# Optimization experiments

Hardware: AMD Instinct MI355X
Metric: run time of the kernel (lower is better)

Reference implementation:

```python
import jax, jax.numpy as jnp
import numpy as np

B, T, C, H = 2, 2048, 1024, 16
D = C // H  # head_dim = 64

def setup_inputs() -> dict:
    key = jax.random.key(0)
    k0, k1, k2, k3, k4 = jax.random.split(key, 5)
    s = 1.0 / np.sqrt(C)
    return {
        "x": jax.random.normal(k0, (B, T, C), dtype=jnp.float32),
        "w_qkv": jax.random.uniform(k1, (C, 3 * C), jnp.float32, -s, s),
        "b_qkv": jax.random.uniform(k2, (3 * C,), jnp.float32, -s, s),
        "w_proj": jax.random.uniform(k3, (C, C), jnp.float32, -s, s),
        "b_proj": jax.random.uniform(k4, (C,), jnp.float32, -s, s),
    }

def reference(x, w_qkv, b_qkv, w_proj, b_proj):
    Bx, Tx, Cx = x.shape
    qkv = x @ w_qkv + b_qkv                      # [B,T,3C]
    q, k, v = jnp.split(qkv, 3, axis=-1)
    # [B,T,C] -> [B,H,T,D]
    def heads(t):
        return t.reshape(Bx, Tx, H, D).transpose(0, 2, 1, 3)
    q, k, v = heads(q), heads(k), heads(v)
    att = jnp.einsum('bhqd,bhkd->bhqk', q, k) / np.sqrt(D).astype(np.float32)
    causal = jnp.tril(jnp.ones((Tx, Tx), dtype=bool))
    att = jnp.where(causal, att, -jnp.inf)
    att = jax.nn.softmax(att, axis=-1)
    y = jnp.einsum('bhqk,bhkd->bhqd', att, v)    # [B,H,T,D]
    y = y.transpose(0, 2, 1, 3).reshape(Bx, Tx, Cx)
    return y @ w_proj + b_proj
```

## Files before the change

kernel.cpp:

```cpp
#include <hip/hip_runtime.h>

typedef short bf16x8 __attribute__((ext_vector_type(8)));
typedef float f32x4 __attribute__((ext_vector_type(4)));
typedef unsigned short u16;
typedef unsigned short u16x8 __attribute__((ext_vector_type(8)));
typedef unsigned short u16x4 __attribute__((ext_vector_type(4), may_alias));
typedef float f32x4_a __attribute__((ext_vector_type(4), may_alias));

__device__ __forceinline__ u16 f2bf(float f) {
    union { float f; unsigned u; } v; v.f = f;
    unsigned r = v.u + 0x7fffu + ((v.u >> 16) & 1u);
    return (u16)(r >> 16);
}
__device__ __forceinline__ u16 f2bf_rhu(float f) {
    union { float f; unsigned u; } v; v.f = f;
    return (u16)((v.u + 0x8000u) >> 16);
}

__device__ __forceinline__ void gld_lds16(const void* g, void* l) {
    __builtin_amdgcn_global_load_lds(
        (const __attribute__((address_space(1))) void*)g,
        (__attribute__((address_space(3))) void*)l, 16, 0, 0);
}

__global__ __launch_bounds__(256) void prep_kernel(
    const float* __restrict__ x, u16* __restrict__ xb,
    const float* __restrict__ w_qkv, u16* __restrict__ wqkvT,
    const float* __restrict__ w_proj, u16* __restrict__ wprojT) {
    __shared__ float tile[32][33];
    const int b = blockIdx.x, tid = threadIdx.x;
    if (b < 2048) {
        const int i = b * 256 + tid;
        float4 a = ((const float4*)x)[i * 2];
        float4 c = ((const float4*)x)[i * 2 + 1];
        u16x8 h;
        h[0] = f2bf(a.x); h[1] = f2bf(a.y); h[2] = f2bf(a.z); h[3] = f2bf(a.w);
        h[4] = f2bf(c.x); h[5] = f2bf(c.y); h[6] = f2bf(c.z); h[7] = f2bf(c.w);
        *(u16x8*)(xb + (size_t)i * 8) = h;
        return;
    }
    const float* in; u16* out; int N, bx;
    if (b < 5120) { bx = b - 2048; in = w_qkv; out = wqkvT; N = 3072; }
    else          { bx = b - 5120; in = w_proj; out = wprojT; N = 1024; }
    const int nblk = N / 32;
    const int n0 = (bx % nblk) * 32, k0 = (bx / nblk) * 32;
    const int tx = tid & 31, ty = tid >> 5;
#pragma unroll
    for (int i = 0; i < 32; i += 8)
        tile[ty + i][tx] = in[(size_t)(k0 + ty + i) * N + n0 + tx];
    __syncthreads();
#pragma unroll
    for (int i = 0; i < 32; i += 8)
        out[(size_t)(n0 + ty + i) * 1024 + k0 + tx] = f2bf(tile[tx][ty + i]);
}

#define QSCALE 0.180336880f

template <int OUTMODE, int BN>
__global__ __launch_bounds__(256) void gemm_m97(
    const u16* __restrict__ A, const u16* __restrict__ Bt,
    const float* __restrict__ bias, float* __restrict__ Cf,
    u16* __restrict__ Qo, u16* __restrict__ Ko, u16* __restrict__ Vt,
    int M, int N, int K) {
    constexpr int NF = BN / 32;
    __shared__ __align__(16) u16 lA[128 * 64];
    __shared__ __align__(16) u16 lB[BN * 64];

    const int tid = threadIdx.x;
    const int lane = tid & 63, wid = tid >> 6;
    const int wr = wid >> 1, wc = wid & 1;
    const int fr = lane & 15, fq = lane >> 4;
    const int m0 = blockIdx.y * 128, n0 = blockIdx.x * BN;

    const int gsrc = (lane & 7) ^ (lane >> 3);
    const u16* gA0 = A + (size_t)(m0 + (tid >> 3)) * K + gsrc * 8;
    const u16* gB0 = Bt + (size_t)(n0 + (tid >> 3)) * K + gsrc * 8;
    u16* lAw = lA + wid * 512;
    u16* lBw = lB + wid * 512;

    const int r7 = fr & 7;
    const int gk[2] = { ((0 + fq) ^ r7) * 8, ((4 + fq) ^ r7) * 8 };

    f32x4 acc[4][NF];
#pragma unroll
    for (int m = 0; m < 4; m++)
#pragma unroll
        for (int n = 0; n < NF; n++)
#pragma unroll
            for (int r = 0; r < 4; r++) acc[m][n][r] = 0.f;

    for (int k0 = 0; k0 < K; k0 += 64) {
        __syncthreads();
#pragma unroll
        for (int c = 0; c < 4; c++)
            gld_lds16(gA0 + (size_t)(c * 32) * K + k0, lAw + c * 2048);
#pragma unroll
        for (int c = 0; c < BN / 32; c++)
            gld_lds16(gB0 + (size_t)(c * 32) * K + k0, lBw + c * 2048);
        __syncthreads();

#pragma unroll
        for (int kf = 0; kf < 2; kf++) {
            bf16x8 a[4], b[NF];
#pragma unroll
            for (int m = 0; m < 4; m++)
                a[m] = *(const bf16x8*)&lA[(wr * 64 + m * 16 + fr) * 64 + gk[kf]];
#pragma unroll
            for (int n = 0; n < NF; n++)
                b[n] = *(const bf16x8*)&lB[(wc * (BN / 2) + n * 16 + fr) * 64 + gk[kf]];
#pragma unroll
            for (int m = 0; m < 4; m++)
#pragma unroll
                for (int n = 0; n < NF; n++)
                    acc[m][n] = __builtin_amdgcn_mfma_f32_16x16x32_bf16(a[m], b[n], acc[m][n], 0, 0, 0);
        }
    }

#pragma unroll
    for (int m = 0; m < 4; m++) {
#pragma unroll
        for (int n = 0; n < NF; n++) {
            const int row0 = m0 + wr * 64 + m * 16 + fq * 4;
            const int col = n0 + wc * (BN / 2) + n * 16 + fr;
            float v4[4];
#pragma unroll
            for (int r = 0; r < 4; r++) v4[r] = acc[m][n][r] + bias[col];
            if (OUTMODE == 0) {
                const int bb = row0 >> 11, t0 = row0 & 2047;
                const int sec = col >> 10, cc = col & 1023;
                const int h = cc >> 6, d = cc & 63;
                if (sec == 0) {
#pragma unroll
                    for (int r = 0; r < 4; r++)
                        Qo[(((size_t)(bb * 16 + h) * 2048 + t0 + r) << 6) + d] = f2bf(v4[r] * QSCALE);
                } else if (sec == 1) {
#pragma unroll
                    for (int r = 0; r < 4; r++)
                        Ko[(((size_t)(bb * 16 + h) * 2048 + t0 + r) << 6) + d] = f2bf(v4[r]);
                } else {
                    ushort4 p;
                    p.x = f2bf(v4[0]); p.y = f2bf(v4[1]); p.z = f2bf(v4[2]); p.w = f2bf(v4[3]);
                    *(ushort4*)&Vt[(((size_t)(bb * 16 + h) * 64 + d) << 11) + t0] = p;
                }
            } else {
#pragma unroll
                for (int r = 0; r < 4; r++)
                    Cf[(size_t)(row0 + r) * N + col] = v4[r];
            }
        }
    }
}

__global__ __launch_bounds__(256, 4) void attn_kernel(const u16* __restrict__ Q,
                                                      const u16* __restrict__ Kg,
                                                      const u16* __restrict__ Vt,
                                                      u16* __restrict__ O) {
    __shared__ __align__(16) u16 smem[16384];
    u16* lV = smem + 8192;
    u16* lPw;

    const int tid = threadIdx.x;
    const int lane = tid & 63, wid = tid >> 6;
    const int fr = lane & 15, fq = lane >> 4;
    const int kw = wid >> 1, qw = wid & 1;
    lPw = smem + 12288 + wid * 1024;
    const int bh = blockIdx.x & 31;
    const int qi = 31 - (blockIdx.x >> 5);
    const int qb0 = qi * 64;
    const size_t base = (size_t)bh * (2048 * 64);
    const u16* Qp = Q + base;
    const u16* Kp = Kg + base;
    const u16* Vp = Vt + base;

    const int q0w = qb0 + qw * 32;
    bf16x8 qa[2][2];
#pragma unroll
    for (int qg = 0; qg < 2; qg++)
#pragma unroll
        for (int kf = 0; kf < 2; kf++)
            qa[qg][kf] = *(const bf16x8*)&Qp[(size_t)(q0w + qg * 16 + fr) * 64 + kf * 32 + fq * 8];

    bf16x8 vones;
#pragma unroll
    for (int j = 0; j < 8; j++) vones[j] = (short)0x3F80;

    f32x4 o[4][2], lsum[2];
#pragma unroll
    for (int qg = 0; qg < 2; qg++) {
#pragma unroll
        for (int r = 0; r < 4; r++) lsum[qg][r] = 0.f;
#pragma unroll
        for (int dg = 0; dg < 4; dg++)
#pragma unroll
            for (int r = 0; r < 4; r++) o[dg][qg][r] = 0.f;
    }

    const int srow0 = wid * 8 + (lane >> 3);
    const int gsrc = (lane & 7) ^ (lane >> 3);
    const u16* kSrc0 = Kp + (size_t)srow0 * 64 + gsrc * 8;
    const u16* vSrc0 = Vp + ((size_t)srow0 << 11) + gsrc * 8;

    const int r7 = fr & 7;
    const int gk0 = ((0 + fq) ^ r7) * 8;
    const int gk1 = ((4 + fq) ^ r7) * 8;
    const int gkv = ((kw * 4 + fq) ^ r7) * 8;

    const int r4x = (fr & 3) ^ (fr >> 2);

    const int nt = qi + 1;

#define STAGE_K(bufofs, kt0_)                                                   \
    do {                                                                        \
        u16* _lkw = smem + (bufofs) + wid * 512;                                \
        gld_lds16(kSrc0 + (size_t)(kt0_) * 64, _lkw);                           \
        gld_lds16(kSrc0 + (size_t)((kt0_) + 32) * 64, _lkw + 2048);             \
    } while (0)
#define STAGE_V(kt0_)                                                           \
    do {                                                                        \
        u16* _lvw = lV + wid * 512;                                             \
        gld_lds16(vSrc0 + (kt0_), _lvw);                                        \
        gld_lds16(vSrc0 + ((size_t)32 << 11) + (kt0_), _lvw + 2048);            \
    } while (0)

    STAGE_K(0, 0);
    STAGE_V(0);
    asm volatile("s_waitcnt vmcnt(0)" ::: "memory");
    __builtin_amdgcn_s_barrier();

    for (int kt = 0; kt < nt; kt++) {
        const int kt0 = kt << 6;
        const int curofs = (kt & 1) ? 4096 : 0;

        if (kt + 1 < nt) {
            STAGE_K(curofs ^ 4096, kt0 + 64);
            asm volatile("s_waitcnt vmcnt(2)" ::: "memory");
            __builtin_amdgcn_s_barrier();
        } else if (nt > 1) {
            asm volatile("s_waitcnt vmcnt(0)" ::: "memory");
            __builtin_amdgcn_s_barrier();
        }
        const u16* lKc = smem + curofs;

        f32x4 s[2][2];
#pragma unroll
        for (int kg = 0; kg < 2; kg++)
#pragma unroll
            for (int qg = 0; qg < 2; qg++)
#pragma unroll
                for (int r = 0; r < 4; r++) s[kg][qg][r] = 0.f;
        __builtin_amdgcn_s_setprio(1);
#pragma unroll
        for (int kg = 0; kg < 2; kg++) {
            const int krow = (kw * 32 + kg * 16 + fr) * 64;
            bf16x8 kb0 = *(const bf16x8*)&lKc[krow + gk0];
            bf16x8 kb1 = *(const bf16x8*)&lKc[krow + gk1];
#pragma unroll
            for (int qg = 0; qg < 2; qg++) {
                s[kg][qg] = __builtin_amdgcn_mfma_f32_16x16x32_bf16(kb0, qa[qg][0], s[kg][qg], 0, 0, 0);
                s[kg][qg] = __builtin_amdgcn_mfma_f32_16x16x32_bf16(kb1, qa[qg][1], s[kg][qg], 0, 0, 0);
            }
        }
        __builtin_amdgcn_s_setprio(0);

        if (kt == nt - 1) {
#pragma unroll
            for (int kg = 0; kg < 2; kg++) {
                const int kg0 = kt0 + kw * 32 + kg * 16 + fq * 4;
#pragma unroll
                for (int qg = 0; qg < 2; qg++) {
                    const int qg0 = q0w + qg * 16 + fr;
#pragma unroll
                    for (int r = 0; r < 4; r++)
                        if (kg0 + r > qg0) s[kg][qg][r] = -200.f;
                }
            }
        }

#pragma unroll
        for (int kg = 0; kg < 2; kg++)
#pragma unroll
            for (int qg = 0; qg < 2; qg++) {
                const int ql = qg * 16 + fr;
                u16x4 w;
                w[0] = f2bf_rhu(__builtin_amdgcn_exp2f(s[kg][qg][0]));
                w[1] = f2bf_rhu(__builtin_amdgcn_exp2f(s[kg][qg][1]));
                w[2] = f2bf_rhu(__builtin_amdgcn_exp2f(s[kg][qg][2]));
                w[3] = f2bf_rhu(__builtin_amdgcn_exp2f(s[kg][qg][3]));
                const int g = (kg * 2 + (fq >> 1)) ^ r4x;
                *(u16x4*)&lPw[ql * 32 + g * 8 + (fq & 1) * 4] = w;
            }
        asm volatile("" ::: "memory");

        __builtin_amdgcn_s_setprio(1);
        bf16x8 va[4];
#pragma unroll
        for (int dg = 0; dg < 4; dg++)
            va[dg] = *(const bf16x8*)&lV[(dg * 16 + fr) * 64 + gkv];
#pragma unroll
        for (int qg = 0; qg < 2; qg++) {
            const int ql = qg * 16 + fr;
            bf16x8 pb = *(const bf16x8*)&lPw[ql * 32 + (fq ^ r4x) * 8];
            lsum[qg] = __builtin_amdgcn_mfma_f32_16x16x32_bf16(vones, pb, lsum[qg], 0, 0, 0);
#pragma unroll
            for (int dg = 0; dg < 4; dg++)
                o[dg][qg] = __builtin_amdgcn_mfma_f32_16x16x32_bf16(va[dg], pb, o[dg][qg], 0, 0, 0);
        }
        __builtin_amdgcn_s_setprio(0);

        if (kt + 1 < nt) {
            __builtin_amdgcn_s_barrier();
            STAGE_V(kt0 + 64);
        }
    }
#undef STAGE_K
#undef STAGE_V

    __syncthreads();

    float* cmb = (float*)smem;
    float* slab = cmb + (size_t)qw * 2560 + lane * 40;
    if (kw == 1) {
#pragma unroll
        for (int dg = 0; dg < 4; dg++)
#pragma unroll
            for (int qg = 0; qg < 2; qg++)
                *(f32x4_a*)&slab[(dg * 2 + qg) * 4] = o[dg][qg];
#pragma unroll
        for (int qg = 0; qg < 2; qg++)
            *(f32x4_a*)&slab[32 + qg * 4] = lsum[qg];
    }
    __syncthreads();
    if (kw == 0) {
#pragma unroll
        for (int dg = 0; dg < 4; dg++)
#pragma unroll
            for (int qg = 0; qg < 2; qg++) {
                f32x4_a p = *(const f32x4_a*)&slab[(dg * 2 + qg) * 4];
#pragma unroll
                for (int r = 0; r < 4; r++) o[dg][qg][r] += p[r];
            }
#pragma unroll
        for (int qg = 0; qg < 2; qg++) {
            f32x4_a p = *(const f32x4_a*)&slab[32 + qg * 4];
            lsum[qg][0] += p[0];
        }

        const int bb = bh >> 4, hh = bh & 15;
#pragma unroll
        for (int qg = 0; qg < 2; qg++) {
            const float inv = 1.f / lsum[qg][0];
            u16* orow = O + ((size_t)(bb * 2048 + q0w + qg * 16 + fr)) * 1024 + hh * 64 + fq * 4;
#pragma unroll
            for (int dg = 0; dg < 4; dg++) {
                ushort4 h;
                h.x = f2bf(o[dg][qg][0] * inv);
                h.y = f2bf(o[dg][qg][1] * inv);
                h.z = f2bf(o[dg][qg][2] * inv);
                h.w = f2bf(o[dg][qg][3] * inv);
                *(ushort4*)&orow[dg * 16] = h;
            }
        }
    }
}

extern "C" void kernel_launch(void* const* d_in, const int* in_sizes, int n_in,
                              void* d_out, int out_size, void* d_ws, size_t ws_size,
                              hipStream_t stream) {
    const float* x      = (const float*)d_in[0];
    const float* w_qkv  = (const float*)d_in[1];
    const float* b_qkv  = (const float*)d_in[2];
    const float* w_proj = (const float*)d_in[3];
    const float* b_proj = (const float*)d_in[4];
    float* out = (float*)d_out;

    u16* ws = (u16*)d_ws;
    u16* wqkvT  = ws;
    u16* wprojT = wqkvT + 3072 * 1024;
    u16* Qb     = wprojT + 1024 * 1024;
    u16* Kb     = Qb + 32 * 2048 * 64;
    u16* Vtb    = Kb + 32 * 2048 * 64;
    u16* xb     = Vtb + 32 * 2048 * 64;
    u16* attnO  = xb;

    prep_kernel<<<6144, 256, 0, stream>>>(x, xb, w_qkv, wqkvT, w_proj, wprojT);

    gemm_m97<0, 128><<<dim3(24, 32), 256, 0, stream>>>(
        xb, wqkvT, b_qkv, nullptr, Qb, Kb, Vtb, 4096, 3072, 1024);

    attn_kernel<<<1024, 256, 0, stream>>>(Qb, Kb, Vtb, attnO);

    gemm_m97<1, 64><<<dim3(16, 32), 256, 0, stream>>>(
        attnO, wprojT, b_proj, out, nullptr, nullptr, nullptr, 4096, 1024, 1024);
}
```

Baseline: 97.05 us.

## Build P operand with permlane swaps and move w_proj transpose into attention tail

The softmax probabilities are now repacked into the MFMA B-operand in registers using v_permlane32/16_swap instead of a round trip through per-wave LDS. This cuts LDS use from 32KB to 24KB, and launch bounds are raised to allow 5 blocks per CU. The w_proj transpose/convert moves out of the prep kernel into 1024 extra blocks appended to the attention launch, which shortens the prep kernel and fills the attention tail. The risks are extra permlane instructions, register pressure under the tighter occupancy bound, and the correctness of the lane permutation.

Measured after the change: 116.8 us. +20.3%, slower.

```diff
diff --git a/kernel.cpp b/kernel.cpp
--- a/kernel.cpp
+++ b/kernel.cpp
@@ -4,7 +4,6 @@
 typedef float f32x4 __attribute__((ext_vector_type(4)));
 typedef unsigned short u16;
 typedef unsigned short u16x8 __attribute__((ext_vector_type(8)));
-typedef unsigned short u16x4 __attribute__((ext_vector_type(4), may_alias));
 typedef float f32x4_a __attribute__((ext_vector_type(4), may_alias));
 
 __device__ __forceinline__ u16 f2bf(float f) {
@@ -25,8 +24,7 @@
 
 __global__ __launch_bounds__(256) void prep_kernel(
     const float* __restrict__ x, u16* __restrict__ xb,
-    const float* __restrict__ w_qkv, u16* __restrict__ wqkvT,
-    const float* __restrict__ w_proj, u16* __restrict__ wprojT) {
+    const float* __restrict__ w_qkv, u16* __restrict__ wqkvT) {
     __shared__ float tile[32][33];
     const int b = blockIdx.x, tid = threadIdx.x;
     if (b < 2048) {
@@ -39,19 +37,16 @@
         *(u16x8*)(xb + (size_t)i * 8) = h;
         return;
     }
-    const float* in; u16* out; int N, bx;
-    if (b < 5120) { bx = b - 2048; in = w_qkv; out = wqkvT; N = 3072; }
-    else          { bx = b - 5120; in = w_proj; out = wprojT; N = 1024; }
-    const int nblk = N / 32;
-    const int n0 = (bx % nblk) * 32, k0 = (bx / nblk) * 32;
+    const int bx = b - 2048;
+    const int n0 = (bx % 96) * 32, k0 = (bx / 96) * 32;
     const int tx = tid & 31, ty = tid >> 5;
 #pragma unroll
     for (int i = 0; i < 32; i += 8)
-        tile[ty + i][tx] = in[(size_t)(k0 + ty + i) * N + n0 + tx];
+        tile[ty + i][tx] = w_qkv[(size_t)(k0 + ty + i) * 3072 + n0 + tx];
     __syncthreads();
 #pragma unroll
     for (int i = 0; i < 32; i += 8)
-        out[(size_t)(n0 + ty + i) * 1024 + k0 + tx] = f2bf(tile[tx][ty + i]);
+        wqkvT[(size_t)(n0 + ty + i) * 1024 + k0 + tx] = f2bf(tile[tx][ty + i]);
 }
 
 #define QSCALE 0.180336880f
@@ -151,19 +146,35 @@
     }
 }
 
-__global__ __launch_bounds__(256, 4) void attn_kernel(const u16* __restrict__ Q,
+__global__ __launch_bounds__(256, 5) void attn_kernel(const u16* __restrict__ Q,
                                                       const u16* __restrict__ Kg,
                                                       const u16* __restrict__ Vt,
-                                                      u16* __restrict__ O) {
-    __shared__ __align__(16) u16 smem[16384];
+                                                      u16* __restrict__ O,
+                                                      const float* __restrict__ wp,
+                                                      u16* __restrict__ wpT) {
+    __shared__ __align__(16) u16 smem[12288];
+
+    const int tid = threadIdx.x;
+
+    if (blockIdx.x >= 1024) {
+        float* tile = (float*)smem;
+        const int bx = blockIdx.x - 1024;
+        const int n0 = (bx & 31) * 32, k0 = (bx >> 5) * 32;
+        const int tx = tid & 31, ty = tid >> 5;
+#pragma unroll
+        for (int i = 0; i < 32; i += 8)
+            tile[(ty + i) * 33 + tx] = wp[(size_t)(k0 + ty + i) * 1024 + n0 + tx];
+        __syncthreads();
+#pragma unroll
+        for (int i = 0; i < 32; i += 8)
+            wpT[(size_t)(n0 + ty + i) * 1024 + k0 + tx] = f2bf(tile[tx * 33 + ty + i]);
+        return;
+    }
+
     u16* lV = smem + 8192;
-    u16* lPw;
-
-    const int tid = threadIdx.x;
     const int lane = tid & 63, wid = tid >> 6;
     const int fr = lane & 15, fq = lane >> 4;
     const int kw = wid >> 1, qw = wid & 1;
-    lPw = smem + 12288 + wid * 1024;
     const int bh = blockIdx.x & 31;
     const int qi = 31 - (blockIdx.x >> 5);
     const int qb0 = qi * 64;
@@ -204,8 +215,6 @@
     const int gk0 = ((0 + fq) ^ r7) * 8;
     const int gk1 = ((4 + fq) ^ r7) * 8;
     const int gkv = ((kw * 4 + fq) ^ r7) * 8;
-
-    const int r4x = (fr & 3) ^ (fr >> 2);
 
     const int nt = qi + 1;
 
@@ -276,36 +285,36 @@
             }
         }
 
-#pragma unroll
-        for (int kg = 0; kg < 2; kg++)
-#pragma unroll
-            for (int qg = 0; qg < 2; qg++) {
-                const int ql = qg * 16 + fr;
-                u16x4 w;
-                w[0] = f2bf_rhu(__builtin_amdgcn_exp2f(s[kg][qg][0]));
-                w[1] = f2bf_rhu(__builtin_amdgcn_exp2f(s[kg][qg][1]));
-                w[2] = f2bf_rhu(__builtin_amdgcn_exp2f(s[kg][qg][2]));
-                w[3] = f2bf_rhu(__builtin_amdgcn_exp2f(s[kg][qg][3]));
-                const int g = (kg * 2 + (fq >> 1)) ^ r4x;
-                *(u16x4*)&lPw[ql * 32 + g * 8 + (fq & 1) * 4] = w;
-            }
-        asm volatile("" ::: "memory");
-
-        __builtin_amdgcn_s_setprio(1);
         bf16x8 va[4];
 #pragma unroll
         for (int dg = 0; dg < 4; dg++)
             va[dg] = *(const bf16x8*)&lV[(dg * 16 + fr) * 64 + gkv];
+
 #pragma unroll
         for (int qg = 0; qg < 2; qg++) {
-            const int ql = qg * 16 + fr;
-            bf16x8 pb = *(const bf16x8*)&lPw[ql * 32 + (fq ^ r4x) * 8];
+            unsigned pa = (unsigned)f2bf_rhu(__builtin_amdgcn_exp2f(s[0][qg][0])) |
+                          ((unsigned)f2bf_rhu(__builtin_amdgcn_exp2f(s[0][qg][1])) << 16);
+            unsigned pb_ = (unsigned)f2bf_rhu(__builtin_amdgcn_exp2f(s[0][qg][2])) |
+                           ((unsigned)f2bf_rhu(__builtin_amdgcn_exp2f(s[0][qg][3])) << 16);
+            unsigned pc = (unsigned)f2bf_rhu(__builtin_amdgcn_exp2f(s[1][qg][0])) |
+                          ((unsigned)f2bf_rhu(__builtin_amdgcn_exp2f(s[1][qg][1])) << 16);
+            unsigned pd = (unsigned)f2bf_rhu(__builtin_amdgcn_exp2f(s[1][qg][2])) |
+                          ((unsigned)f2bf_rhu(__builtin_amdgcn_exp2f(s[1][qg][3])) << 16);
+            asm("v_permlane32_swap_b32 %0, %1" : "+v"(pa), "+v"(pc));
+            asm("v_permlane16_swap_b32 %0, %1" : "+v"(pa), "+v"(pc));
+            asm("v_permlane32_swap_b32 %0, %1" : "+v"(pb_), "+v"(pd));
+            asm("v_permlane16_swap_b32 %0, %1" : "+v"(pb_), "+v"(pd));
+            union { unsigned u[4]; bf16x8 v; } pbu;
+            pbu.u[0] = pa; pbu.u[1] = pb_; pbu.u[2] = pc; pbu.u[3] = pd;
+            const bf16x8 pb = pbu.v;
+
+            __builtin_amdgcn_s_setprio(1);
             lsum[qg] = __builtin_amdgcn_mfma_f32_16x16x32_bf16(vones, pb, lsum[qg], 0, 0, 0);
 #pragma unroll
             for (int dg = 0; dg < 4; dg++)
                 o[dg][qg] = __builtin_amdgcn_mfma_f32_16x16x32_bf16(va[dg], pb, o[dg][qg], 0, 0, 0);
-        }
-        __builtin_amdgcn_s_setprio(0);
+            __builtin_amdgcn_s_setprio(0);
+        }
 
         if (kt + 1 < nt) {
             __builtin_amdgcn_s_barrier();
@@ -382,12 +391,12 @@
     u16* xb     = Vtb + 32 * 2048 * 64;
     u16* attnO  = xb;
 
-    prep_kernel<<<6144, 256, 0, stream>>>(x, xb, w_qkv, wqkvT, w_proj, wprojT);
+    prep_kernel<<<5120, 256, 0, stream>>>(x, xb, w_qkv, wqkvT);
 
     gemm_m97<0, 128><<<dim3(24, 32), 256, 0, stream>>>(
         xb, wqkvT, b_qkv, nullptr, Qb, Kb, Vtb, 4096, 3072, 1024);
 
-    attn_kernel<<<1024, 256, 0, stream>>>(Qb, Kb, Vtb, attnO);
+    attn_kernel<<<2048, 256, 0, stream>>>(Qb, Kb, Vtb, attnO, w_proj, wprojT);
 
     gemm_m97<1, 64><<<dim3(16, 32), 256, 0, stream>>>(
         attnO, wprojT, b_proj, out, nullptr, nullptr, nullptr, 4096, 1024, 1024);
```
